# Kernel tuning notes

Measured on AMD Instinct MI355X. Metric: run time of the kernel, lower is better.

Reference implementation:

```python
import math
import jax, jax.numpy as jnp
import numpy as np

TAU = 2.0
ALPHA = math.exp(-1.0 / TAU)
SCALE = 1.0

T, B, H, N, D = 16, 16, 8, 256, 64


def setup_inputs() -> dict:
    key = jax.random.key(0)
    x = jax.random.normal(key, (T, B, H, N, D), dtype=jnp.float32)
    return {"x": x}


def reference(x):
    # state_t = alpha * state_{t-1} + x_t  (state_0-init = 0)
    # out_t   = x_t * sigmoid(scale * state_t)
    def step(state, xt):
        state = ALPHA * state + xt
        return state, xt * jax.nn.sigmoid(SCALE * state)

    init = jnp.zeros_like(x[0])  # [B, H, N, D]
    _, out = jax.lax.scan(step, init, x)  # out: [T, B, H, N, D]
    return out
```

## Files before the change

### kernel.cpp

```cpp
#include <hip/hip_runtime.h>


#define T_STEPS 16
#define SPATIAL (16LL * 8LL * 256LL * 64LL)
#define VEC4    (SPATIAL / 4)
#define ALPHA_F 0.60653065971263342f
#define SUB     8

typedef float f32x4 __attribute__((ext_vector_type(4)));

__global__ __launch_bounds__(256) void
TemporalPSPGate_35613868819159_kernel(const f32x4* __restrict__ x,
                                      f32x4* __restrict__ out) {
    const int tid  = threadIdx.x;
    const int wave = tid >> 6;
    const int lane = tid & 63;
    const long long wb = ((long long)blockIdx.x * 4 + wave) * (64 * SUB);
    const long long j  = wb + lane;

    f32x4 bufA[SUB], bufB[SUB], xt[SUB], st[SUB];

    #pragma unroll
    for (int s = 0; s < SUB; ++s)
        bufA[s] = __builtin_nontemporal_load(x + j + 64 * s);
    #pragma unroll
    for (int s = 0; s < SUB; ++s)
        bufB[s] = __builtin_nontemporal_load(x + VEC4 + j + 64 * s);
    #pragma unroll
    for (int s = 0; s < SUB; ++s) st[s] = (f32x4){0.f, 0.f, 0.f, 0.f};

    #define STEP(T, CURBUF)                                                   \
    {                                                                         \
        _Pragma("unroll")                                                     \
        for (int s = 0; s < SUB; ++s) xt[s] = CURBUF[s];                      \
        if ((T) + 2 < T_STEPS) {                                              \
            _Pragma("unroll")                                                 \
            for (int s = 0; s < SUB; ++s)                                     \
                CURBUF[s] = __builtin_nontemporal_load(                       \
                    x + (long long)((T) + 2) * VEC4 + j + 64 * s);            \
        }                                                                     \
        _Pragma("unroll")                                                     \
        for (int s = 0; s < SUB; ++s) {                                       \
            st[s] = ALPHA_F * st[s] + xt[s];                                  \
            f32x4 o;                                                          \
            _Pragma("unroll")                                                 \
            for (int c = 0; c < 4; ++c) {                                     \
                const float e = __expf(-st[s][c]);                            \
                o[c] = xt[s][c] * __builtin_amdgcn_rcpf(1.0f + e);            \
            }                                                                 \
            out[(long long)(T) * VEC4 + j + 64 * s] = o;                      \
        }                                                                     \
    }

    #pragma unroll
    for (int tt = 0; tt < T_STEPS; tt += 2) {
        STEP(tt,     bufA);
        STEP(tt + 1, bufB);
    }
    #undef STEP
}

extern "C" void kernel_launch(void* const* d_in, const int* in_sizes, int n_in,
                              void* d_out, int out_size, void* d_ws, size_t ws_size,
                              hipStream_t stream) {
    const f32x4* x = (const f32x4*)d_in[0];
    f32x4* out = (f32x4*)d_out;

    const int block = 256;
    const int grid = (int)(VEC4 / (block * SUB));

    TemporalPSPGate_35613868819159_kernel<<<grid, block, 0, stream>>>(x, out);
}
```

Before: 231.4 us.

## Halve spatial width per thread and deepen temporal prefetch to four steps

Each thread now covers 4 spatial vectors instead of 8, but its buffers hold two timesteps each, so loads are issued four timesteps ahead instead of two. The grid doubles while the number of loads in flight per thread stays the same. Stores are grouped after the compute of each two-step chunk. This is meant to give more waves and deeper temporal lookahead to hide memory latency, in exchange for similar register pressure and a different store ordering.

New measurement: 217.1 us. 6.2% less time.

```diff
diff --git a/kernel.cpp b/kernel.cpp
--- a/kernel.cpp
+++ b/kernel.cpp
@@ -5,7 +5,7 @@
 #define SPATIAL (16LL * 8LL * 256LL * 64LL)
 #define VEC4    (SPATIAL / 4)
 #define ALPHA_F 0.60653065971263342f
-#define SUB     8
+#define SUB     4
 
 typedef float f32x4 __attribute__((ext_vector_type(4)));
 
@@ -18,46 +18,53 @@
     const long long wb = ((long long)blockIdx.x * 4 + wave) * (64 * SUB);
     const long long j  = wb + lane;
 
-    f32x4 bufA[SUB], bufB[SUB], xt[SUB], st[SUB];
+    f32x4 bufA[8], bufB[8], xt[8], st[SUB];
 
     #pragma unroll
-    for (int s = 0; s < SUB; ++s)
-        bufA[s] = __builtin_nontemporal_load(x + j + 64 * s);
+    for (int q = 0; q < 8; ++q)
+        bufA[q] = __builtin_nontemporal_load(
+            x + (long long)(q >> 2) * VEC4 + j + 64 * (q & 3));
     #pragma unroll
-    for (int s = 0; s < SUB; ++s)
-        bufB[s] = __builtin_nontemporal_load(x + VEC4 + j + 64 * s);
+    for (int q = 0; q < 8; ++q)
+        bufB[q] = __builtin_nontemporal_load(
+            x + (long long)(2 + (q >> 2)) * VEC4 + j + 64 * (q & 3));
     #pragma unroll
     for (int s = 0; s < SUB; ++s) st[s] = (f32x4){0.f, 0.f, 0.f, 0.f};
 
-    #define STEP(T, CURBUF)                                                   \
+    #define SSTEP(TT, BUF)                                                    \
     {                                                                         \
         _Pragma("unroll")                                                     \
-        for (int s = 0; s < SUB; ++s) xt[s] = CURBUF[s];                      \
-        if ((T) + 2 < T_STEPS) {                                              \
+        for (int q = 0; q < 8; ++q) xt[q] = BUF[q];                           \
+        if ((TT) + 4 < T_STEPS) {                                             \
             _Pragma("unroll")                                                 \
-            for (int s = 0; s < SUB; ++s)                                     \
-                CURBUF[s] = __builtin_nontemporal_load(                       \
-                    x + (long long)((T) + 2) * VEC4 + j + 64 * s);            \
+            for (int q = 0; q < 8; ++q)                                       \
+                BUF[q] = __builtin_nontemporal_load(                          \
+                    x + (long long)((TT) + 4 + (q >> 2)) * VEC4               \
+                      + j + 64 * (q & 3));                                    \
         }                                                                     \
+        f32x4 o[8];                                                           \
         _Pragma("unroll")                                                     \
-        for (int s = 0; s < SUB; ++s) {                                       \
-            st[s] = ALPHA_F * st[s] + xt[s];                                  \
-            f32x4 o;                                                          \
+        for (int q = 0; q < 8; ++q) {                                         \
+            const int s = q & 3;    \
+            st[s] = ALPHA_F * st[s] + xt[q];                                  \
             _Pragma("unroll")                                                 \
             for (int c = 0; c < 4; ++c) {                                     \
                 const float e = __expf(-st[s][c]);                            \
-                o[c] = xt[s][c] * __builtin_amdgcn_rcpf(1.0f + e);            \
+                o[q][c] = xt[q][c] * __builtin_amdgcn_rcpf(1.0f + e);         \
             }                                                                 \
-            out[(long long)(T) * VEC4 + j + 64 * s] = o;                      \
         }                                                                     \
+        _Pragma("unroll")                                                     \
+        for (int q = 0; q < 8; ++q)                                           \
+            out[(long long)((TT) + (q >> 2)) * VEC4 + j + 64 * (q & 3)]       \
+                = o[q];                                                       \
     }
 
     #pragma unroll
-    for (int tt = 0; tt < T_STEPS; tt += 2) {
-        STEP(tt,     bufA);
-        STEP(tt + 1, bufB);
+    for (int tt = 0; tt < T_STEPS; tt += 4) {
+        SSTEP(tt,     bufA);
+        SSTEP(tt + 2, bufB);
     }
-    #undef STEP
+    #undef SSTEP
 }
 
 extern "C" void kernel_launch(void* const* d_in, const int* in_sizes, int n_in,
```
